# Performance work log

Hardware: AMD Instinct MI355X
Metric: run time of the kernel (lower is better)

The kernel has to match this reference:

```python
import jax, jax.numpy as jnp
import numpy as np

EMBED_DIM = 1024
BATCH = 4
SEQ = 2048


def setup_inputs() -> dict:
    key = jax.random.key(0)
    ks = jax.random.split(key, 9)
    E = EMBED_DIM
    s = 1.0 / np.sqrt(E)
    inp = {
        "x": jax.random.normal(ks[0], (BATCH, SEQ, E), dtype=jnp.float32),
        "Wq": jax.random.uniform(ks[1], (E, E), jnp.float32, -s, s),
        "bq": jax.random.uniform(ks[2], (E,), jnp.float32, -s, s),
        "Wk": jax.random.uniform(ks[3], (E, E), jnp.float32, -s, s),
        "bk": jax.random.uniform(ks[4], (E,), jnp.float32, -s, s),
        "Wv": jax.random.uniform(ks[5], (E, E), jnp.float32, -s, s),
        "bv": jax.random.uniform(ks[6], (E,), jnp.float32, -s, s),
        "Wo": jax.random.uniform(ks[7], (E, E), jnp.float32, -s, s),
        "bo": jax.random.uniform(ks[8], (E,), jnp.float32, -s, s),
    }
    return inp


def reference(x, Wq, bq, Wk, bk, Wv, bv, Wo, bo):
    # x: [B, S, E]. Single-head attention over full embed_dim.
    scale = x.shape[-1] ** -0.5
    q = jnp.einsum("bse,ef->bsf", x, Wq.T) + bq
    k = jnp.einsum("bse,ef->bsf", x, Wk.T) + bk
    v = jnp.einsum("bse,ef->bsf", x, Wv.T) + bv
    scores = jnp.einsum("bqe,bke->bqk", q, k) * scale  # [B, S, S]
    attn = jax.nn.softmax(scores, axis=-1)             # dropout p=0 -> identity
    out = jnp.einsum("bqk,bke->bqe", attn, v)
    return jnp.einsum("bse,ef->bsf", out, Wo.T) + bo
```

## Files before the change

### kernel.cpp

```cpp
#include <hip/hip_runtime.h>
#include <hip/hip_bf16.h>


typedef __bf16 bf16_t;
typedef __bf16 bf16x8 __attribute__((ext_vector_type(8)));
typedef __bf16 bf16x4 __attribute__((ext_vector_type(4)));
typedef float  f32x16 __attribute__((ext_vector_type(16)));

__device__ __forceinline__ void async_copy16(const void* g, void* l) {
  __builtin_amdgcn_global_load_lds(
      (const __attribute__((address_space(1))) void*)g,
      (__attribute__((address_space(3))) void*)l, 16, 0, 0);
}

__device__ __forceinline__ void store_out(float* p, float v)  { *p = v; }
__device__ __forceinline__ void store_out(bf16_t* p, float v) { *p = (bf16_t)v; }

#define BM 128
#define BN 128
#define BKT 64

template <typename OutT, int NBIAS>
__global__ __launch_bounds__(256) void gemm_bt(
    const bf16_t* __restrict__ A, const bf16_t* __restrict__ B,
    OutT* __restrict__ C,
    const float* __restrict__ b0, const float* __restrict__ b1,
    const float* __restrict__ b2,
    int M, int N, int K, int lda, int ldb, int ldc, float scale,
    long long strideA, long long strideB, long long strideC) {
  const int z = blockIdx.z;
  A += (long long)z * strideA;
  B += (long long)z * strideB;
  C += (long long)z * strideC;

  __shared__ __align__(16) bf16_t As[BM * BKT];
  __shared__ __align__(16) bf16_t Bs[BN * BKT];

  const int t    = threadIdx.x;
  const int lane = t & 63;
  const int w    = t >> 6;
  const int wm   = w & 1;
  const int wn   = w >> 1;
  const int tileM = blockIdx.y * BM;
  const int tileN = blockIdx.x * BN;

  f32x16 acc[2][2] = {};

  for (int k0 = 0; k0 < K; k0 += BKT) {
#pragma unroll
    for (int i = 0; i < 4; ++i) {
      const int c   = t + 256 * i;
      const int row = c >> 3;
      const int cc  = c & 7;
      const int gcc = (cc + 3 * row) & 7;
      const int ldsbase = ((t & ~63) + 256 * i) * 8;
      async_copy16(A + (long long)(tileM + row) * lda + k0 + gcc * 8, &As[ldsbase]);
      async_copy16(B + (long long)(tileN + row) * ldb + k0 + gcc * 8, &Bs[ldsbase]);
    }
    __syncthreads();

#pragma unroll
    for (int s = 0; s < 4; ++s) {
      const int kc = s * 2 + (lane >> 5);
      bf16x8 af[2], bfr[2];
#pragma unroll
      for (int ti = 0; ti < 2; ++ti) {
        const int row = wm * 64 + ti * 32 + (lane & 31);
        af[ti] = *(const bf16x8*)&As[row * BKT + (((kc + 5 * row) & 7) * 8)];
      }
#pragma unroll
      for (int tj = 0; tj < 2; ++tj) {
        const int row = wn * 64 + tj * 32 + (lane & 31);
        bfr[tj] = *(const bf16x8*)&Bs[row * BKT + (((kc + 5 * row) & 7) * 8)];
      }
#pragma unroll
      for (int ti = 0; ti < 2; ++ti)
#pragma unroll
        for (int tj = 0; tj < 2; ++tj)
          acc[ti][tj] = __builtin_amdgcn_mfma_f32_32x32x16_bf16(
              af[ti], bfr[tj], acc[ti][tj], 0, 0, 0);
    }
    __syncthreads();
  }

#pragma unroll
  for (int tj = 0; tj < 2; ++tj) {
    const int col = tileN + wn * 64 + tj * 32 + (lane & 31);
    float bv = 0.f;
    if (NBIAS == 1) bv = b0[col];
    if (NBIAS == 3) {
      const float* bp = col < 1024 ? b0 : (col < 2048 ? b1 : b2);
      bv = bp[col & 1023];
    }
#pragma unroll
    for (int ti = 0; ti < 2; ++ti) {
      const int rowb = tileM + wm * 64 + ti * 32 + 4 * (lane >> 5);
#pragma unroll
      for (int r = 0; r < 16; ++r) {
        const int row = rowb + (r & 3) + 8 * (r >> 2);
        store_out(&C[(long long)row * ldc + col], acc[ti][tj][r] * scale + bv);
      }
    }
  }
}

__global__ __launch_bounds__(256) void cast_weights(
    const float4* __restrict__ w0, const float4* __restrict__ w1,
    const float4* __restrict__ w2, const float4* __restrict__ w3,
    bf16x4* __restrict__ dst, int n4) {
  const int z = blockIdx.z;
  const float4* src = z == 0 ? w0 : (z == 1 ? w1 : (z == 2 ? w2 : w3));
  const int i = blockIdx.x * 256 + threadIdx.x;
  if (i >= n4) return;
  const float4 v = src[i];
  bf16x4 o;
  o[0] = (bf16_t)v.x; o[1] = (bf16_t)v.y; o[2] = (bf16_t)v.z; o[3] = (bf16_t)v.w;
  dst[(long long)z * n4 + i] = o;
}

__global__ __launch_bounds__(256) void cast_f32_bf16(
    const float4* __restrict__ in, bf16x4* __restrict__ out, int n4) {
  const int i = blockIdx.x * 256 + threadIdx.x;
  if (i >= n4) return;
  const float4 v = in[i];
  bf16x4 o;
  o[0] = (bf16_t)v.x; o[1] = (bf16_t)v.y; o[2] = (bf16_t)v.z; o[3] = (bf16_t)v.w;
  out[i] = o;
}

__global__ __launch_bounds__(256) void transpose_bf16(
    const bf16_t* __restrict__ in, bf16_t* __restrict__ out, int R, int C,
    int ldin, long long sIn, long long sOut) {
  in  += (long long)blockIdx.z * sIn;
  out += (long long)blockIdx.z * sOut;
  __shared__ bf16_t tile[32][33];
  const int tx = threadIdx.x, ty = threadIdx.y;
  const int x = blockIdx.x * 32 + tx;
  const int y0 = blockIdx.y * 32;
#pragma unroll
  for (int j = 0; j < 32; j += 8)
    tile[ty + j][tx] = in[(long long)(y0 + ty + j) * ldin + x];
  __syncthreads();
  const int x2 = y0 + tx;
  const int y2 = blockIdx.x * 32;
#pragma unroll
  for (int j = 0; j < 32; j += 8)
    out[(long long)(y2 + ty + j) * R + x2] = tile[tx][ty + j];
}

__global__ __launch_bounds__(256) void softmax_rows(
    const bf16_t* __restrict__ S, bf16_t* __restrict__ P, int cols) {
  const long long row = blockIdx.x;
  const bf16x8* inp = (const bf16x8*)(S + row * cols);
  bf16x8* outp      = (bf16x8*)(P + row * cols);
  const int t = threadIdx.x;
  const int w = t >> 6, lane = t & 63;

  const bf16x8 v = inp[t];
  float f[8];
#pragma unroll
  for (int j = 0; j < 8; ++j) f[j] = (float)v[j];

  float m = f[0];
#pragma unroll
  for (int j = 1; j < 8; ++j) m = fmaxf(m, f[j]);
#pragma unroll
  for (int off = 32; off > 0; off >>= 1) m = fmaxf(m, __shfl_xor(m, off));

  __shared__ float red[8];
  if (lane == 0) red[w] = m;
  __syncthreads();
  m = fmaxf(fmaxf(red[0], red[1]), fmaxf(red[2], red[3]));

  float e[8], sum = 0.f;
#pragma unroll
  for (int j = 0; j < 8; ++j) { e[j] = __expf(f[j] - m); sum += e[j]; }
#pragma unroll
  for (int off = 32; off > 0; off >>= 1) sum += __shfl_xor(sum, off);
  if (lane == 0) red[4 + w] = sum;
  __syncthreads();
  sum = red[4] + red[5] + red[6] + red[7];

  const float inv = 1.f / sum;
  bf16x8 o;
#pragma unroll
  for (int j = 0; j < 8; ++j) o[j] = (bf16_t)(e[j] * inv);
  outp[t] = o;
}

extern "C" void kernel_launch(void* const* d_in, const int* in_sizes, int n_in,
                              void* d_out, int out_size, void* d_ws, size_t ws_size,
                              hipStream_t stream) {
  const int E = 1024, S = 2048, B = 4;
  const int BS = B * S;

  const float* x  = (const float*)d_in[0];
  const float* Wq = (const float*)d_in[1];
  const float* bq = (const float*)d_in[2];
  const float* Wk = (const float*)d_in[3];
  const float* bk = (const float*)d_in[4];
  const float* Wv = (const float*)d_in[5];
  const float* bv = (const float*)d_in[6];
  const float* Wo = (const float*)d_in[7];
  const float* bo = (const float*)d_in[8];
  float* out = (float*)d_out;

  char* w = (char*)d_ws;
  const size_t MB = 1ull << 20;
  bf16_t* Wqkvb = (bf16_t*)(w + 0 * MB);
  bf16_t* Wob   = Wqkvb + 3 * E * E;
  bf16_t* xb    = (bf16_t*)(w + 8 * MB);
  bf16_t* QKVb  = (bf16_t*)(w + 24 * MB);
  bf16_t* VTb   = (bf16_t*)(w + 72 * MB);
  bf16_t* Sb    = (bf16_t*)(w + 88 * MB);
  bf16_t* Pb    = (bf16_t*)(w + 8 * MB);
  bf16_t* Ob    = (bf16_t*)(w + 40 * MB);

  const int n4w = E * E / 4;
  cast_weights<<<dim3((n4w + 255) / 256, 1, 4), 256, 0, stream>>>(
      (const float4*)Wq, (const float4*)Wk, (const float4*)Wv, (const float4*)Wo,
      (bf16x4*)Wqkvb, n4w);
  const int n4x = BS * E / 4;
  cast_f32_bf16<<<(n4x + 255) / 256, 256, 0, stream>>>(
      (const float4*)x, (bf16x4*)xb, n4x);

  gemm_bt<bf16_t, 3><<<dim3(3 * E / BN, BS / BM, 1), 256, 0, stream>>>(
      xb, Wqkvb, QKVb, bq, bk, bv,
      BS, 3 * E, E, E, E, 3 * E, 1.f, 0, 0, 0);

  transpose_bf16<<<dim3(E / 32, S / 32, B), dim3(32, 8), 0, stream>>>(
      QKVb + 2 * E, VTb, S, E, 3 * E, (long long)S * 3 * E, (long long)E * S);

  gemm_bt<bf16_t, 0><<<dim3(S / BN, S / BM, B), 256, 0, stream>>>(
      QKVb, QKVb + E, Sb, nullptr, nullptr, nullptr,
      S, S, E, 3 * E, 3 * E, S, 0.03125f,
      (long long)S * 3 * E, (long long)S * 3 * E, (long long)S * S);

  softmax_rows<<<BS, 256, 0, stream>>>(Sb, Pb, S);

  gemm_bt<bf16_t, 0><<<dim3(E / BN, S / BM, B), 256, 0, stream>>>(
      Pb, VTb, Ob, nullptr, nullptr, nullptr,
      S, E, S, S, S, E, 1.f,
      (long long)S * S, (long long)E * S, (long long)S * E);

  gemm_bt<float, 1><<<dim3(E / BN, BS / BM, 1), 256, 0, stream>>>(
      Ob, Wob, out, bo, nullptr, nullptr,
      BS, E, E, E, E, E, 1.f, 0, 0, 0);
}
```

Measured before the change: 302.4 us.

## Swizzle GEMM block order, change LDS swizzle, merge cast kernels

The GEMM kernel remaps block indices into groups of 8 row-tiles so that concurrently running blocks share A/B panels in L2. The LDS chunk swizzle is changed so each half-wave reads from a separate 4-slot half, with rotation by row, to reduce bank conflicts. The weight and activation cast kernels are merged into one launch to cut launch overhead. The grouping assumes gridDim.y is a multiple of 8, which holds for all current launches.

```diff
diff --git a/kernel.cpp b/kernel.cpp
--- a/kernel.cpp
+++ b/kernel.cpp
@@ -33,6 +33,17 @@
   B += (long long)z * strideB;
   C += (long long)z * strideC;
 
+  int bx = blockIdx.x, by = blockIdx.y;
+  {
+    const int GX  = gridDim.x;
+    const int id  = by * GX + bx;
+    const int per = GX * 8;
+    const int grp = id / per;
+    const int rem = id - grp * per;
+    by = grp * 8 + (rem & 7);
+    bx = rem >> 3;
+  }
+
   __shared__ __align__(16) bf16_t As[BM * BKT];
   __shared__ __align__(16) bf16_t Bs[BN * BKT];
 
@@ -41,8 +52,8 @@
   const int w    = t >> 6;
   const int wm   = w & 1;
   const int wn   = w >> 1;
-  const int tileM = blockIdx.y * BM;
-  const int tileN = blockIdx.x * BN;
+  const int tileM = by * BM;
+  const int tileN = bx * BN;
 
   f32x16 acc[2][2] = {};
 
@@ -52,7 +63,7 @@
       const int c   = t + 256 * i;
       const int row = c >> 3;
       const int cc  = c & 7;
-      const int gcc = (cc + 3 * row) & 7;
+      const int gcc = ((((cc & 3) - row) & 3) << 1) | (cc >> 2);
       const int ldsbase = ((t & ~63) + 256 * i) * 8;
       async_copy16(A + (long long)(tileM + row) * lda + k0 + gcc * 8, &As[ldsbase]);
       async_copy16(B + (long long)(tileN + row) * ldb + k0 + gcc * 8, &Bs[ldsbase]);
@@ -61,17 +72,19 @@
 
 #pragma unroll
     for (int s = 0; s < 4; ++s) {
-      const int kc = s * 2 + (lane >> 5);
+      const int h = lane >> 5;
       bf16x8 af[2], bfr[2];
 #pragma unroll
       for (int ti = 0; ti < 2; ++ti) {
         const int row = wm * 64 + ti * 32 + (lane & 31);
-        af[ti] = *(const bf16x8*)&As[row * BKT + (((kc + 5 * row) & 7) * 8)];
+        const int slot = 4 * h + ((s + row) & 3);
+        af[ti] = *(const bf16x8*)&As[row * BKT + slot * 8];
       }
 #pragma unroll
       for (int tj = 0; tj < 2; ++tj) {
         const int row = wn * 64 + tj * 32 + (lane & 31);
-        bfr[tj] = *(const bf16x8*)&Bs[row * BKT + (((kc + 5 * row) & 7) * 8)];
+        const int slot = 4 * h + ((s + row) & 3);
+        bfr[tj] = *(const bf16x8*)&Bs[row * BKT + slot * 8];
       }
 #pragma unroll
       for (int ti = 0; ti < 2; ++ti)
@@ -104,28 +117,28 @@
   }
 }
 
-__global__ __launch_bounds__(256) void cast_weights(
+__global__ __launch_bounds__(256) void cast_all(
     const float4* __restrict__ w0, const float4* __restrict__ w1,
     const float4* __restrict__ w2, const float4* __restrict__ w3,
-    bf16x4* __restrict__ dst, int n4) {
-  const int z = blockIdx.z;
-  const float4* src = z == 0 ? w0 : (z == 1 ? w1 : (z == 2 ? w2 : w3));
-  const int i = blockIdx.x * 256 + threadIdx.x;
-  if (i >= n4) return;
-  const float4 v = src[i];
+    const float4* __restrict__ x,
+    bf16x4* __restrict__ wdst, bf16x4* __restrict__ xdst) {
+  const int N4W = 1 << 18;
+  const int id = blockIdx.x * 256 + threadIdx.x;
+  const float4* src;
+  bf16x4* dst;
+  if (id < 4 * N4W) {
+    const int z = id >> 18;
+    src = (z == 0 ? w0 : z == 1 ? w1 : z == 2 ? w2 : w3) + (id & (N4W - 1));
+    dst = wdst + id;
+  } else {
+    const int i = id - 4 * N4W;
+    src = x + i;
+    dst = xdst + i;
+  }
+  const float4 v = *src;
   bf16x4 o;
   o[0] = (bf16_t)v.x; o[1] = (bf16_t)v.y; o[2] = (bf16_t)v.z; o[3] = (bf16_t)v.w;
-  dst[(long long)z * n4 + i] = o;
-}
-
-__global__ __launch_bounds__(256) void cast_f32_bf16(
-    const float4* __restrict__ in, bf16x4* __restrict__ out, int n4) {
-  const int i = blockIdx.x * 256 + threadIdx.x;
-  if (i >= n4) return;
-  const float4 v = in[i];
-  bf16x4 o;
-  o[0] = (bf16_t)v.x; o[1] = (bf16_t)v.y; o[2] = (bf16_t)v.z; o[3] = (bf16_t)v.w;
-  out[i] = o;
+  *dst = o;
 }
 
 __global__ __launch_bounds__(256) void transpose_bf16(
@@ -216,13 +229,12 @@
   bf16_t* Pb    = (bf16_t*)(w + 8 * MB);
   bf16_t* Ob    = (bf16_t*)(w + 40 * MB);
 
-  const int n4w = E * E / 4;
-  cast_weights<<<dim3((n4w + 255) / 256, 1, 4), 256, 0, stream>>>(
-      (const float4*)Wq, (const float4*)Wk, (const float4*)Wv, (const float4*)Wo,
-      (bf16x4*)Wqkvb, n4w);
-  const int n4x = BS * E / 4;
-  cast_f32_bf16<<<(n4x + 255) / 256, 256, 0, stream>>>(
-      (const float4*)x, (bf16x4*)xb, n4x);
+  {
+    const int totalBlocks = ((4 << 18) + (1 << 21)) / 256;
+    cast_all<<<totalBlocks, 256, 0, stream>>>(
+        (const float4*)Wq, (const float4*)Wk, (const float4*)Wv,
+        (const float4*)Wo, (const float4*)x, (bf16x4*)Wqkvb, (bf16x4*)xb);
+  }
 
   gemm_bt<bf16_t, 3><<<dim3(3 * E / BN, BS / BM, 1), 256, 0, stream>>>(
       xb, Wqkvb, QKVb, bq, bk, bv,
```

Result: slower. 317.0 us (+4.8%).
